# Performance work log

Hardware: AMD Instinct MI355X
Metric: run time of the kernel (lower is better)

Reference implementation:

```python
import jax, jax.numpy as jnp
import numpy as np

N_NODES = 100000
N_EDGES = 1600000
N_GRAPHS = 256
IN_DIM, HID = 30, 40

def setup_inputs() -> dict:
    key = jax.random.key(0)
    ks = jax.random.split(key, 12)
    x = jax.random.normal(ks[0], (N_NODES, IN_DIM), dtype=jnp.float32)
    edge_index = jax.random.randint(ks[1], (2, N_EDGES), 0, N_NODES, dtype=jnp.int64)
    batch = jnp.sort(jax.random.randint(ks[2], (N_NODES,), 0, N_GRAPHS, dtype=jnp.int64))
    def glorot(k, shape):
        lim = float(np.sqrt(6.0 / (shape[0] + shape[1])))
        return jax.random.uniform(k, shape, dtype=jnp.float32, minval=-lim, maxval=lim)
    return {
        'x': x, 'edge_index': edge_index, 'batch': batch,
        'W1': glorot(ks[3], (IN_DIM, HID)), 'b1': jnp.zeros((HID,), jnp.float32),
        'W2': glorot(ks[4], (HID, HID)),    'b2': jnp.zeros((HID,), jnp.float32),
        'W3': glorot(ks[5], (HID, HID)),    'b3': jnp.zeros((HID,), jnp.float32),
        'lin_w': glorot(ks[6], (HID, 1)),   'lin_b': jnp.zeros((1,), jnp.float32),
    }

def _gcn_layer(x, src, dst, norm, W, b, n_nodes):
    # x: [N, Fin] -> [N, Fout]; fused gather-matmul-scatter form of GCNConv
    h = x @ W                                   # dense transform first (Fout small)
    msg = h[src] * norm[:, None]                # [E+N, Fout] gather + edge scale
    out = jax.ops.segment_sum(msg, dst, num_segments=n_nodes)
    return out + b

def reference(x, edge_index, batch, W1, b1, W2, b2, W3, b3, lin_w, lin_b):
    n = x.shape[0]
    loops = jnp.arange(n, dtype=edge_index.dtype)
    src = jnp.concatenate([edge_index[0], loops])  # add self loops (GCNConv default)
    dst = jnp.concatenate([edge_index[1], loops])
    deg = jax.ops.segment_sum(jnp.ones_like(dst, dtype=x.dtype), dst, num_segments=n)
    dinv = jax.lax.rsqrt(jnp.maximum(deg, 1.0))    # deg >= 1 thanks to self loops
    norm = dinv[src] * dinv[dst]

    h = jax.nn.relu(_gcn_layer(x, src, dst, norm, W1, b1, n))  # dropout inactive (eval)
    h = jax.nn.relu(_gcn_layer(h, src, dst, norm, W2, b2, n))
    h = jax.nn.relu(_gcn_layer(h, src, dst, norm, W3, b3, n))

    # global_mean_pool over graphs
    g_sum = jax.ops.segment_sum(h, batch, num_segments=N_GRAPHS)
    cnt = jax.ops.segment_sum(jnp.ones((n,), h.dtype), batch, num_segments=N_GRAPHS)
    g = g_sum / jnp.maximum(cnt, 1.0)[:, None]
    return g @ lin_w + lin_b                      # [N_GRAPHS, 1]
```

## Files before the change

kernel.cpp:

```cpp
#include <hip/hip_runtime.h>

#define HID 40
#define RBKT 196
#define BSH 9
#define CAP 12288
#define EPB 4096


typedef __attribute__((ext_vector_type(4))) unsigned uv4;
typedef __attribute__((ext_vector_type(8))) __bf16 bf16x8;
typedef __attribute__((ext_vector_type(8))) unsigned short usv8;
typedef __attribute__((ext_vector_type(4))) float f32x4;

__device__ inline unsigned pack2_bf16(float a, float b) {
    unsigned ua = __float_as_uint(a);
    unsigned ub = __float_as_uint(b);
    ua = (ua + 0x7fffu + ((ua >> 16) & 1u)) >> 16;
    ub = (ub + 0x7fffu + ((ub >> 16) & 1u)) & 0xffff0000u;
    return ua | ub;
}

__device__ inline void acc8_bf16(float* acc, uint4 v) {
    acc[0] += __uint_as_float(v.x << 16);
    acc[1] += __uint_as_float(v.x & 0xffff0000u);
    acc[2] += __uint_as_float(v.y << 16);
    acc[3] += __uint_as_float(v.y & 0xffff0000u);
    acc[4] += __uint_as_float(v.z << 16);
    acc[5] += __uint_as_float(v.z & 0xffff0000u);
    acc[6] += __uint_as_float(v.w << 16);
    acc[7] += __uint_as_float(v.w & 0xffff0000u);
}

__device__ inline void wprep_dev(const float* __restrict__ W,
                                 unsigned* __restrict__ wtab, int INF, int l) {
    int lr = l & 15, lg = l >> 4;
    int kstn = (INF > 32) ? 2 : 1;
    for (int kst = 0; kst < kstn; kst++) {
        for (int ct = 0; ct < 3; ct++) {
            unsigned short v[8];
            #pragma unroll
            for (int i = 0; i < 8; i++) {
                int kb = kst * 32 + lg * 8 + i;
                int col = ct * 16 + lr;
                float f = (kb < INF && col < 40) ? W[kb * 40 + col] : 0.f;
                v[i] = (unsigned short)(pack2_bf16(f, 0.f) & 0xffffu);
            }
            uint4 u;
            u.x = (unsigned)v[0] | ((unsigned)v[1] << 16);
            u.y = (unsigned)v[2] | ((unsigned)v[3] << 16);
            u.z = (unsigned)v[4] | ((unsigned)v[5] << 16);
            u.w = (unsigned)v[6] | ((unsigned)v[7] << 16);
            reinterpret_cast<uint4*>(wtab)[(kst * 3 + ct) * 64 + l] = u;
        }
    }
}

__global__ void prep_kernel(int* __restrict__ bucket_cnt, float* __restrict__ g_sum, int G,
                            const float* __restrict__ W1, const float* __restrict__ W2,
                            const float* __restrict__ W3,
                            unsigned* __restrict__ wtab1, unsigned* __restrict__ wtab2,
                            unsigned* __restrict__ wtab3) {
    int t = threadIdx.x;
    if (t < RBKT) bucket_cnt[t] = 0;
    if (t < G) g_sum[t] = 0.f;
    int w = t >> 6, l = t & 63;
    if (w == 1) wprep_dev(W1, wtab1, 30, l);
    else if (w == 2) wprep_dev(W2, wtab2, 40, l);
    else if (w == 3) wprep_dev(W3, wtab3, 40, l);
}


__global__ __launch_bounds__(256) void binA_kernel(
        const int* __restrict__ esrc, const int* __restrict__ edst, int E,
        int* __restrict__ bucket_cnt, int* __restrict__ bucket_data) {
    __shared__ int cnt_l[RBKT];
    __shared__ int base_l[RBKT];
    int t = threadIdx.x;
    for (int b = t; b < RBKT; b += 256) cnt_l[b] = 0;
    __syncthreads();
    int e0 = blockIdx.x * EPB;
    int e1 = min(e0 + EPB, E);
    for (int e = e0 + t; e < e1; e += 256) {
        atomicAdd(&cnt_l[edst[e] >> BSH], 1);
    }
    __syncthreads();
    for (int b = t; b < RBKT; b += 256) {
        int c = cnt_l[b];
        base_l[b] = (c > 0) ? atomicAdd(&bucket_cnt[b], c) : 0;
        cnt_l[b] = 0;
    }
    __syncthreads();
    for (int e = e0 + t; e < e1; e += 256) {
        int d = edst[e];
        int s = esrc[e];
        int b = d >> BSH;
        int off = base_l[b] + atomicAdd(&cnt_l[b], 1);
        if (off < CAP) bucket_data[(size_t)b * CAP + off] = (s << BSH) | (d & 511);
    }
}

__global__ void scan_buckets_kernel(const int* __restrict__ cnt, int* __restrict__ base) {
    __shared__ int s[256];
    int t = threadIdx.x;
    int c = (t < RBKT) ? min(cnt[t], CAP) : 0;
    s[t] = c;
    __syncthreads();
    for (int off = 1; off < 256; off <<= 1) {
        int y = (t >= off) ? s[t - off] : 0;
        __syncthreads();
        s[t] += y;
        __syncthreads();
    }
    if (t < RBKT) base[t] = s[t] - c;
    if (t == RBKT - 1) base[RBKT] = s[t];
}

__global__ __launch_bounds__(256) void buildB_kernel(
        const int* __restrict__ bucket_cnt, const int* __restrict__ bucket_base,
        const int* __restrict__ bucket_data,
        int* __restrict__ rowptr, int* __restrict__ mid, int* __restrict__ csr,
        float* __restrict__ dinv, int n, int half) {
    __shared__ int deg_l[512];
    __shared__ int deg_lo[512];
    __shared__ int off_lo[512];
    __shared__ int off_hi[512];
    __shared__ int ps[256];
    int r = blockIdx.x;
    int t = threadIdx.x;
    int cnt = min(bucket_cnt[r], CAP);
    int base = bucket_base[r];
    int node0 = r << BSH;
    int nr = min(512, n - node0);
    for (int i = t; i < 512; i += 256) { deg_l[i] = 0; deg_lo[i] = 0; }
    __syncthreads();
    const int* data = bucket_data + (size_t)r * CAP;
    for (int e = t; e < cnt; e += 256) {
        int v = data[e];
        atomicAdd(&deg_l[v & 511], 1);
        if ((v >> BSH) < half) atomicAdd(&deg_lo[v & 511], 1);
    }
    __syncthreads();
    int a0 = deg_l[2 * t], a1 = deg_l[2 * t + 1];
    ps[t] = a0 + a1;
    __syncthreads();
    for (int off = 1; off < 256; off <<= 1) {
        int y = (t >= off) ? ps[t - off] : 0;
        __syncthreads();
        ps[t] += y;
        __syncthreads();
    }
    int excl = ps[t] - (a0 + a1);
    off_lo[2 * t] = excl;
    off_lo[2 * t + 1] = excl + a0;
    off_hi[2 * t] = excl + deg_lo[2 * t];
    off_hi[2 * t + 1] = excl + a0 + deg_lo[2 * t + 1];
    __syncthreads();
    for (int i = t; i < nr; i += 256) {
        int rp = base + off_lo[i];
        rowptr[node0 + i] = rp;
        mid[node0 + i] = rp + deg_lo[i];
        dinv[node0 + i] = rsqrtf((float)(deg_l[i] + 1));
    }
    if (r == RBKT - 1 && t == 0) rowptr[n] = base + cnt;
    __syncthreads();
    for (int e = t; e < cnt; e += 256) {
        int v = data[e];
        int s = v >> BSH;
        int d = v & 511;
        int p = (s < half) ? atomicAdd(&off_lo[d], 1) : atomicAdd(&off_hi[d], 1);
        csr[base + p] = s;
    }
}


__global__ __launch_bounds__(256) void scale_bf16_kernel(
        const float* __restrict__ x, const float* __restrict__ dinv,
        unsigned* __restrict__ xs, int n) {
    int t = blockIdx.x * blockDim.x + threadIdx.x;
    int i = t >> 4, p = t & 15;
    if (i >= n) return;
    float a = 0.f, b = 0.f;
    if (p < 15) {
        float d = dinv[i];
        a = x[i * 30 + 2 * p] * d;
        b = x[i * 30 + 2 * p + 1] * d;
    }
    xs[(size_t)i * 16 + p] = pack2_bf16(a, b);
}

template <int INF, int RQ, bool POOL>
__global__ __launch_bounds__(64 * RQ) void fused_layer_kernel(
        const unsigned* __restrict__ xs, const unsigned* __restrict__ wtab,
        const int* __restrict__ rowptr, const int* __restrict__ mid,
        const int* __restrict__ csr, const float* __restrict__ dinv,
        const float* __restrict__ bias, const float* __restrict__ lin_w,
        const int* __restrict__ batch,
        unsigned* __restrict__ out, float* __restrict__ g_sum, int n) {
    constexpr int KST = (INF > 32) ? 2 : 1;
    constexpr int TS  = (RQ == 4) ? 5 : 7;
    __shared__ uint4 tile[64 * TS];
    __shared__ float sarr[POOL ? 64 : 1];
    const int tid = threadIdx.x;
    const uint4* tab = reinterpret_cast<const uint4*>(xs);

    {
        const int node_l = tid / RQ, q = tid - node_l * RQ;
        const int gi = blockIdx.x * 64 + node_l;
        if (gi < n) {
            float acc[8];
            {
                uint4 v = tab[(size_t)gi * RQ + q];
                acc[0] = __uint_as_float(v.x << 16);
                acc[1] = __uint_as_float(v.x & 0xffff0000u);
                acc[2] = __uint_as_float(v.y << 16);
                acc[3] = __uint_as_float(v.y & 0xffff0000u);
                acc[4] = __uint_as_float(v.z << 16);
                acc[5] = __uint_as_float(v.z & 0xffff0000u);
                acc[6] = __uint_as_float(v.w << 16);
                acc[7] = __uint_as_float(v.w & 0xffff0000u);
            }
            int e0 = rowptr[gi], m = mid[gi], e1 = rowptr[gi + 1];
            int e = e0;
            for (; e + 4 <= m; e += 4) {
                int s0 = csr[e], s1 = csr[e + 1], s2 = csr[e + 2], s3 = csr[e + 3];
                uint4 v0 = tab[(size_t)s0 * RQ + q];
                uint4 v1 = tab[(size_t)s1 * RQ + q];
                uint4 v2 = tab[(size_t)s2 * RQ + q];
                uint4 v3 = tab[(size_t)s3 * RQ + q];
                acc8_bf16(acc, v0);
                acc8_bf16(acc, v1);
                acc8_bf16(acc, v2);
                acc8_bf16(acc, v3);
            }
            for (; e < m; e++) acc8_bf16(acc, tab[(size_t)csr[e] * RQ + q]);
            for (; e + 4 <= e1; e += 4) {
                int s0 = csr[e], s1 = csr[e + 1], s2 = csr[e + 2], s3 = csr[e + 3];
                uint4 v0 = tab[(size_t)s0 * RQ + q];
                uint4 v1 = tab[(size_t)s1 * RQ + q];
                uint4 v2 = tab[(size_t)s2 * RQ + q];
                uint4 v3 = tab[(size_t)s3 * RQ + q];
                acc8_bf16(acc, v0);
                acc8_bf16(acc, v1);
                acc8_bf16(acc, v2);
                acc8_bf16(acc, v3);
            }
            for (; e < e1; e++) acc8_bf16(acc, tab[(size_t)csr[e] * RQ + q]);
            float d = dinv[gi];
            uint4 o;
            o.x = pack2_bf16(acc[0] * d, acc[1] * d);
            o.y = pack2_bf16(acc[2] * d, acc[3] * d);
            o.z = pack2_bf16(acc[4] * d, acc[5] * d);
            o.w = pack2_bf16(acc[6] * d, acc[7] * d);
            tile[node_l * TS + q] = o;
        }
    }
    __syncthreads();

    const int wv = tid >> 6, l = tid & 63, lr = l & 15, lg = l >> 4;
    if (wv < 4) {
        const uv4* wt = reinterpret_cast<const uv4*>(wtab);
        usv8 wf[KST][3];
        #pragma unroll
        for (int kst = 0; kst < KST; kst++) {
            #pragma unroll
            for (int ct = 0; ct < 3; ct++) {
                wf[kst][ct] = __builtin_bit_cast(usv8, wt[(kst * 3 + ct) * 64 + l]);
            }
        }
        const int node0 = blockIdx.x * 64 + wv * 16;
        const int arow_l = wv * 16 + lr;
        bf16x8 a0 = __builtin_bit_cast(bf16x8, tile[arow_l * TS + lg]);
        bf16x8 a1;
        if constexpr (KST == 2) {
            uint4 z4 = {0u, 0u, 0u, 0u};
            uint4 a1q = (lg == 0) ? tile[arow_l * TS + 4] : z4;
            a1 = __builtin_bit_cast(bf16x8, a1q);
        }
        f32x4 acc[3];
        #pragma unroll
        for (int ct = 0; ct < 3; ct++) {
            f32x4 z = {0.f, 0.f, 0.f, 0.f};
            acc[ct] = __builtin_amdgcn_mfma_f32_16x16x32_bf16(
                a0, __builtin_bit_cast(bf16x8, wf[0][ct]), z, 0, 0, 0);
            if constexpr (KST == 2) {
                acc[ct] = __builtin_amdgcn_mfma_f32_16x16x32_bf16(
                    a1, __builtin_bit_cast(bf16x8, wf[1][ct]), acc[ct], 0, 0, 0);
            }
        }
        int noder[4]; float dr[4]; bool vr[4];
        #pragma unroll
        for (int r = 0; r < 4; r++) {
            noder[r] = node0 + lg * 4 + r;
            vr[r] = (noder[r] < n);
            dr[r] = vr[r] ? dinv[noder[r]] : 0.f;
        }
        if (!POOL) {
            #pragma unroll
            for (int ct = 0; ct < 3; ct++) {
                int col = ct * 16 + lr;
                float bc = (col < 40) ? bias[col] : 0.f;
                #pragma unroll
                for (int r = 0; r < 4; r++) {
                    float v = fmaxf(acc[ct][r] + bc, 0.f) * dr[r];
                    float pv = __shfl_xor(v, 1, 64);
                    if (((lr & 1) == 0) && vr[r] && col < 40) {
                        out[(size_t)noder[r] * 20 + ct * 8 + (lr >> 1)] = pack2_bf16(v, pv);
                    }
                }
            }
        } else {
            float s[4] = {0.f, 0.f, 0.f, 0.f};
            #pragma unroll
            for (int ct = 0; ct < 3; ct++) {
                int col = ct * 16 + lr;
                float bc = (col < 40) ? bias[col] : 0.f;
                float lwv = (col < 40) ? lin_w[col] : 0.f;
                #pragma unroll
                for (int r = 0; r < 4; r++)
                    s[r] += fmaxf(acc[ct][r] + bc, 0.f) * lwv;
            }
            #pragma unroll
            for (int r = 0; r < 4; r++) if (!vr[r]) s[r] = 0.f;
            #pragma unroll
            for (int mask = 1; mask <= 8; mask <<= 1) {
                #pragma unroll
                for (int r = 0; r < 4; r++) s[r] += __shfl_xor(s[r], mask, 64);
            }
            if (lr == 0) {
                #pragma unroll
                for (int r = 0; r < 4; r++) sarr[wv * 16 + lg * 4 + r] = s[r];
            }
        }
    }
    if (POOL) {
        __syncthreads();
        if (tid < 64) {
            float ss = sarr[tid];
            int node2 = blockIdx.x * 64 + tid;
            bool v2 = (node2 < n);
            int gg = batch[v2 ? node2 : (n - 1)];
            if (!v2) ss = 0.f;
            int g0 = __shfl(gg, 0, 64);
            if (__all(gg == g0)) {
                #pragma unroll
                for (int off2 = 32; off2 > 0; off2 >>= 1) ss += __shfl_xor(ss, off2, 64);
                if (tid == 0) atomicAdd(&g_sum[g0], ss);
            } else {
                if (v2) atomicAdd(&g_sum[gg], ss);
            }
        }
    }
}

__global__ void finalize_kernel(const float* __restrict__ g_sum,
                                const int* __restrict__ batch,
                                const float* __restrict__ lin_b,
                                float* __restrict__ out, int n, int G) {
    int b = blockIdx.x * blockDim.x + threadIdx.x;
    if (b >= G) return;
    int lo = 0, hi = n;
    while (lo < hi) { int m = (lo + hi) >> 1; if (batch[m] < b) lo = m + 1; else hi = m; }
    int lo2 = lo, hi2 = n;
    while (lo2 < hi2) { int m = (lo2 + hi2) >> 1; if (batch[m] < b + 1) lo2 = m + 1; else hi2 = m; }
    int cnt = lo2 - lo;
    out[b] = g_sum[b] / (float)(cnt > 0 ? cnt : 1) + lin_b[0];
}


static inline size_t align_up(size_t v, size_t a) { return (v + a - 1) / a * a; }

extern "C" void kernel_launch(void* const* d_in, const int* in_sizes, int n_in,
                              void* d_out, int out_size, void* d_ws, size_t ws_size,
                              hipStream_t stream) {
    const float* x      = (const float*)d_in[0];
    const int*   esrc   = (const int*)d_in[1];
    const int*   batch  = (const int*)d_in[2];
    const float* W1     = (const float*)d_in[3];
    const float* b1     = (const float*)d_in[4];
    const float* W2     = (const float*)d_in[5];
    const float* b2     = (const float*)d_in[6];
    const float* W3     = (const float*)d_in[7];
    const float* b3     = (const float*)d_in[8];
    const float* lin_w  = (const float*)d_in[9];
    const float* lin_b  = (const float*)d_in[10];
    float* out = (float*)d_out;

    const int n = in_sizes[0] / 30;
    const int E = in_sizes[1] / 2;
    const int G = out_size;
    const int* edst = esrc + E;

    char* w = (char*)d_ws;
    size_t off = 0;
    auto take = [&](size_t bytes) { size_t o = off; off = align_up(off + bytes, 256); return (void*)(w + o); };
    int*      bucket_cnt  = (int*)take((size_t)RBKT * 4);
    int*      bucket_base = (int*)take((size_t)(RBKT + 1) * 4);
    int*      rowptr      = (int*)take((size_t)(n + 1) * 4);
    int*      mid         = (int*)take((size_t)n * 4);
    float*    dinv        = (float*)take((size_t)n * 4);
    int*      csr         = (int*)take((size_t)E * 4);
    float*    g_sum       = (float*)take((size_t)G * 4);
    unsigned* wtab1       = (unsigned*)take((size_t)3 * 64 * 16);
    unsigned* wtab2       = (unsigned*)take((size_t)6 * 64 * 16);
    unsigned* wtab3       = (unsigned*)take((size_t)6 * 64 * 16);
    size_t bd = (size_t)RBKT * CAP * 4;
    size_t x1 = (size_t)n * 16 * 4;
    void* shared_region = take(bd > x1 ? bd : x1);
    int*      bucket_data = (int*)shared_region;
    unsigned* xs1         = (unsigned*)shared_region;
    unsigned* tbA         = (unsigned*)take((size_t)n * 20 * 4);
    unsigned* tbB         = (unsigned*)take((size_t)n * 20 * 4);
    (void)ws_size;

    prep_kernel<<<1, 256, 0, stream>>>(bucket_cnt, g_sum, G, W1, W2, W3,
                                       wtab1, wtab2, wtab3);

    binA_kernel<<<(E + EPB - 1) / EPB, 256, 0, stream>>>(esrc, edst, E, bucket_cnt, bucket_data);
    scan_buckets_kernel<<<1, 256, 0, stream>>>(bucket_cnt, bucket_base);
    buildB_kernel<<<RBKT, 256, 0, stream>>>(bucket_cnt, bucket_base, bucket_data,
                                            rowptr, mid, csr, dinv, n, n / 2);

    int nblk = (n + 63) / 64;

    scale_bf16_kernel<<<((size_t)n * 16 + 255) / 256, 256, 0, stream>>>(x, dinv, xs1, n);
    fused_layer_kernel<30, 4, false><<<nblk, 256, 0, stream>>>(
        xs1, wtab1, rowptr, mid, csr, dinv, b1, nullptr, nullptr, tbA, nullptr, n);
    fused_layer_kernel<40, 5, false><<<nblk, 320, 0, stream>>>(
        tbA, wtab2, rowptr, mid, csr, dinv, b2, nullptr, nullptr, tbB, nullptr, n);
    fused_layer_kernel<40, 5, true><<<nblk, 320, 0, stream>>>(
        tbB, wtab3, rowptr, mid, csr, dinv, b3, lin_w, batch, nullptr, g_sum, n);

    finalize_kernel<<<1, 256, 0, stream>>>(g_sum, batch, lin_b, out, n, G);
}
```

Before: 199.0 us.

## Reorder nodes by graph and degree within buckets to balance gather wavefronts

buildB now computes, per 512-node bucket, a permutation that sorts nodes by (graph id offset, clamped degree) with a counting sort. The fused layer kernels process nodes in that permuted order, so lanes in a wavefront have similar edge counts and less divergence in the gather loop, while pooling stays mostly within one graph. The cost is extra indirection loads of nperm in each layer, less sequential access to the rowptr and output rows, and extra work in buildB.

```diff
diff --git a/kernel.cpp b/kernel.cpp
--- a/kernel.cpp
+++ b/kernel.cpp
@@ -117,9 +117,9 @@
 
 __global__ __launch_bounds__(256) void buildB_kernel(
         const int* __restrict__ bucket_cnt, const int* __restrict__ bucket_base,
-        const int* __restrict__ bucket_data,
+        const int* __restrict__ bucket_data, const int* __restrict__ batch,
         int* __restrict__ rowptr, int* __restrict__ mid, int* __restrict__ csr,
-        float* __restrict__ dinv, int n, int half) {
+        float* __restrict__ dinv, int* __restrict__ nperm, int n, int half) {
     __shared__ int deg_l[512];
     __shared__ int deg_lo[512];
     __shared__ int off_lo[512];
@@ -131,6 +131,7 @@
     int base = bucket_base[r];
     int node0 = r << BSH;
     int nr = min(512, n - node0);
+    if (nr <= 0) return;
     for (int i = t; i < 512; i += 256) { deg_l[i] = 0; deg_lo[i] = 0; }
     __syncthreads();
     const int* data = bucket_data + (size_t)r * CAP;
@@ -169,6 +170,33 @@
         int d = v & 511;
         int p = (s < half) ? atomicAdd(&off_lo[d], 1) : atomicAdd(&off_hi[d], 1);
         csr[base + p] = s;
+    }
+    __syncthreads();
+    for (int i = t; i < 512; i += 256) off_lo[i] = 0;
+    __syncthreads();
+    int gbase = batch[node0];
+    for (int i = t; i < nr; i += 256) {
+        int key = min(batch[node0 + i] - gbase, 7) * 64 + min(deg_l[i], 63);
+        deg_lo[i] = key;
+        atomicAdd(&off_lo[key], 1);
+    }
+    __syncthreads();
+    int c0 = off_lo[2 * t], c1 = off_lo[2 * t + 1];
+    ps[t] = c0 + c1;
+    __syncthreads();
+    for (int off = 1; off < 256; off <<= 1) {
+        int y = (t >= off) ? ps[t - off] : 0;
+        __syncthreads();
+        ps[t] += y;
+        __syncthreads();
+    }
+    int ex2 = ps[t] - (c0 + c1);
+    off_hi[2 * t] = ex2;
+    off_hi[2 * t + 1] = ex2 + c0;
+    __syncthreads();
+    for (int i = t; i < nr; i += 256) {
+        int p = atomicAdd(&off_hi[deg_lo[i]], 1);
+        nperm[node0 + p] = node0 + i;
     }
 }
 
@@ -193,6 +221,7 @@
         const unsigned* __restrict__ xs, const unsigned* __restrict__ wtab,
         const int* __restrict__ rowptr, const int* __restrict__ mid,
         const int* __restrict__ csr, const float* __restrict__ dinv,
+        const int* __restrict__ nperm,
         const float* __restrict__ bias, const float* __restrict__ lin_w,
         const int* __restrict__ batch,
         unsigned* __restrict__ out, float* __restrict__ g_sum, int n) {
@@ -205,8 +234,9 @@
 
     {
         const int node_l = tid / RQ, q = tid - node_l * RQ;
-        const int gi = blockIdx.x * 64 + node_l;
-        if (gi < n) {
+        const int j = blockIdx.x * 64 + node_l;
+        if (j < n) {
+            const int gi = nperm[j];
             float acc[8];
             {
                 uint4 v = tab[(size_t)gi * RQ + q];
@@ -267,7 +297,6 @@
                 wf[kst][ct] = __builtin_bit_cast(usv8, wt[(kst * 3 + ct) * 64 + l]);
             }
         }
-        const int node0 = blockIdx.x * 64 + wv * 16;
         const int arow_l = wv * 16 + lr;
         bf16x8 a0 = __builtin_bit_cast(bf16x8, tile[arow_l * TS + lg]);
         bf16x8 a1;
@@ -290,8 +319,9 @@
         int noder[4]; float dr[4]; bool vr[4];
         #pragma unroll
         for (int r = 0; r < 4; r++) {
-            noder[r] = node0 + lg * 4 + r;
-            vr[r] = (noder[r] < n);
+            int jg = blockIdx.x * 64 + wv * 16 + lg * 4 + r;
+            vr[r] = (jg < n);
+            noder[r] = vr[r] ? nperm[jg] : 0;
             dr[r] = vr[r] ? dinv[noder[r]] : 0.f;
         }
         if (!POOL) {
@@ -336,8 +366,9 @@
         __syncthreads();
         if (tid < 64) {
             float ss = sarr[tid];
-            int node2 = blockIdx.x * 64 + tid;
-            bool v2 = (node2 < n);
+            int j2 = blockIdx.x * 64 + tid;
+            bool v2 = (j2 < n);
+            int node2 = v2 ? nperm[j2] : 0;
             int gg = batch[v2 ? node2 : (n - 1)];
             if (!v2) ss = 0.f;
             int g0 = __shfl(gg, 0, 64);
@@ -400,6 +431,7 @@
     float*    dinv        = (float*)take((size_t)n * 4);
     int*      csr         = (int*)take((size_t)E * 4);
     float*    g_sum       = (float*)take((size_t)G * 4);
+    int*      nperm       = (int*)take((size_t)n * 4);
     unsigned* wtab1       = (unsigned*)take((size_t)3 * 64 * 16);
     unsigned* wtab2       = (unsigned*)take((size_t)6 * 64 * 16);
     unsigned* wtab3       = (unsigned*)take((size_t)6 * 64 * 16);
@@ -417,18 +449,18 @@
 
     binA_kernel<<<(E + EPB - 1) / EPB, 256, 0, stream>>>(esrc, edst, E, bucket_cnt, bucket_data);
     scan_buckets_kernel<<<1, 256, 0, stream>>>(bucket_cnt, bucket_base);
-    buildB_kernel<<<RBKT, 256, 0, stream>>>(bucket_cnt, bucket_base, bucket_data,
-                                            rowptr, mid, csr, dinv, n, n / 2);
+    buildB_kernel<<<RBKT, 256, 0, stream>>>(bucket_cnt, bucket_base, bucket_data, batch,
+                                            rowptr, mid, csr, dinv, nperm, n, n / 2);
 
     int nblk = (n + 63) / 64;
 
     scale_bf16_kernel<<<((size_t)n * 16 + 255) / 256, 256, 0, stream>>>(x, dinv, xs1, n);
     fused_layer_kernel<30, 4, false><<<nblk, 256, 0, stream>>>(
-        xs1, wtab1, rowptr, mid, csr, dinv, b1, nullptr, nullptr, tbA, nullptr, n);
+        xs1, wtab1, rowptr, mid, csr, dinv, nperm, b1, nullptr, nullptr, tbA, nullptr, n);
     fused_layer_kernel<40, 5, false><<<nblk, 320, 0, stream>>>(
-        tbA, wtab2, rowptr, mid, csr, dinv, b2, nullptr, nullptr, tbB, nullptr, n);
+        tbA, wtab2, rowptr, mid, csr, dinv, nperm, b2, nullptr, nullptr, tbB, nullptr, n);
     fused_layer_kernel<40, 5, true><<<nblk, 320, 0, stream>>>(
-        tbB, wtab3, rowptr, mid, csr, dinv, b3, lin_w, batch, nullptr, g_sum, n);
+        tbB, wtab3, rowptr, mid, csr, dinv, nperm, b3, lin_w, batch, nullptr, g_sum, n);
 
     finalize_kernel<<<1, 256, 0, stream>>>(g_sum, batch, lin_b, out, n, G);
 }
```

New measurement: 209.2 us. 1.05x slower.
